# Optimization experiments

Measured on AMD Instinct MI355X. Metric: run time of the kernel, lower is better.

## Reference

```python
import jax, jax.numpy as jnp
import numpy as np

B, L, S = 128, 400, 30
V, EMB, H, M, OOV = 50000, 128, 512, 512, 30


def setup_inputs():
    ks = jax.random.split(jax.random.key(0), 32)
    rn = lambda k, s, sc=0.05: jax.random.normal(k, s, dtype=jnp.float32) * sc
    return {
        "h": rn(ks[0], (1, B, H), 1.0),
        "word_memory_bank": rn(ks[1], (B, L, M), 1.0),
        "sent_memory_bank": rn(ks[2], (B, S, M), 1.0),
        "src_word_mask": (jax.random.uniform(ks[3], (B, L)) < 0.9).astype(jnp.float32),
        "src_sent_mask": (jax.random.uniform(ks[4], (B, S)) < 0.9).astype(jnp.float32),
        "coverage": jnp.zeros((B, L), jnp.float32),
        "emb_table": rn(ks[5], (V, EMB), 1.0).at[0].set(0.0),  # pad_idx=0 row zeroed
        "gru_w_ih": rn(ks[6], (3 * H, EMB)),
        "gru_w_hh": rn(ks[7], (3 * H, H)),
        "gru_b_ih": rn(ks[8], (3 * H,)),
        "gru_b_hh": rn(ks[9], (3 * H,)),
        "w_mem_proj": rn(ks[10], (H, M)),
        "w_dec_proj_w": rn(ks[11], (H, H)),
        "w_dec_proj_b": rn(ks[12], (H,)),
        "w_v": rn(ks[13], (H,)),
        "w_cov_proj": rn(ks[14], (H,)),
        "s_mem_proj": rn(ks[15], (H, M)),
        "s_dec_proj_w": rn(ks[16], (H, H)),
        "s_dec_proj_b": rn(ks[17], (H,)),
        "s_v": rn(ks[18], (H,)),
        "pgen_w": rn(ks[19], (EMB + H + 2 * M,)),
        "pgen_b": rn(ks[20], (1,)),
        "vd1_w": rn(ks[21], (H, H + 2 * M)),
        "vd1_b": rn(ks[22], (H,)),
        "vd2_w": rn(ks[23], (V, H)),
        "vd2_b": rn(ks[24], (V,)),
        "y": jax.random.randint(ks[25], (B,), 0, V),
        "src_oov": jax.random.randint(ks[26], (B, L), 0, V + OOV),
        "max_num_oovs": OOV,
    }


def _attn_concat(dec, mem, mask, mem_proj, dec_w, dec_b, v, cov=None, cov_proj=None):
    # concat/Bahdanau attention: score = v^T tanh(W_m m + W_d s [+ W_c c])
    feat = jnp.einsum('blm,dm->bld', mem, mem_proj) + (dec @ dec_w.T + dec_b)[:, None, :]
    if cov is not None:
        feat = feat + cov[:, :, None] * cov_proj[None, None, :]
    scores = jnp.einsum('bld,d->bl', jnp.tanh(feat), v)
    attn = jax.nn.softmax(scores, axis=1)
    if mask is not None:  # masked softmax: softmax, mask, renormalize
        attn = attn * mask
        attn = attn / (jnp.sum(attn, axis=1, keepdims=True) + 1e-10)
    ctx = jnp.einsum('bl,blm->bm', attn, mem)
    new_cov = cov + attn if cov is not None else None
    return ctx, attn, new_cov


def _forward(h, word_memory_bank, sent_memory_bank, src_word_mask, src_sent_mask,
             coverage, emb_table, gru_w_ih, gru_w_hh, gru_b_ih, gru_b_hh,
             w_mem_proj, w_dec_proj_w, w_dec_proj_b, w_v, w_cov_proj,
             s_mem_proj, s_dec_proj_w, s_dec_proj_b, s_v,
             pgen_w, pgen_b, vd1_w, vd1_b, vd2_w, vd2_b, y, src_oov, max_num_oovs):
    bsz = src_oov.shape[0]
    y_emb = emb_table[y]  # [B, EMB]
    # single-step GRU (PyTorch gate layout r,z,n)
    gi = y_emb @ gru_w_ih.T + gru_b_ih
    gh = h[-1] @ gru_w_hh.T + gru_b_hh
    ir, iz, inn = jnp.split(gi, 3, axis=1)
    hr, hz, hn = jnp.split(gh, 3, axis=1)
    r = jax.nn.sigmoid(ir + hr)
    z = jax.nn.sigmoid(iz + hz)
    n = jnp.tanh(inn + r * hn)
    h_last = (1.0 - z) * n + z * h[-1]  # [B, H]
    h_next = h_last[None]  # [1, B, H]
    word_ctx, word_attn, word_cov = _attn_concat(
        h_last, word_memory_bank, src_word_mask, w_mem_proj, w_dec_proj_w,
        w_dec_proj_b, w_v, coverage, w_cov_proj)
    sent_ctx, _, _ = _attn_concat(
        h_last, sent_memory_bank, src_sent_mask, s_mem_proj, s_dec_proj_w,
        s_dec_proj_b, s_v)
    context = jnp.concatenate([word_ctx, sent_ctx], axis=1)  # [B, 2M]
    hid = jnp.concatenate([context, h_last], axis=1) @ vd1_w.T + vd1_b
    vocab_dist = jax.nn.softmax(hid @ vd2_w.T + vd2_b, axis=1)  # [B, V]
    pg_in = jnp.concatenate([context, h_last, y_emb], axis=1)
    p_gen = jax.nn.sigmoid(pg_in @ pgen_w + pgen_b)[:, None]  # [B, 1]
    vocab_dist_ = p_gen * vocab_dist
    attn_dist_ = (1.0 - p_gen) * word_attn
    vocab_dist_ = jnp.concatenate(
        [vocab_dist_, jnp.zeros((bsz, max_num_oovs), vocab_dist_.dtype)], axis=1)
    final_dist = vocab_dist_.at[jnp.arange(bsz)[:, None], src_oov].add(attn_dist_)
    return final_dist, h_next, word_ctx, word_attn, p_gen, word_cov


def reference(h, word_memory_bank, sent_memory_bank, src_word_mask, src_sent_mask,
              coverage, emb_table, gru_w_ih, gru_w_hh, gru_b_ih, gru_b_hh,
              w_mem_proj, w_dec_proj_w, w_dec_proj_b, w_v, w_cov_proj,
              s_mem_proj, s_dec_proj_w, s_dec_proj_b, s_v,
              pgen_w, pgen_b, vd1_w, vd1_b, vd2_w, vd2_b, y, src_oov, max_num_oovs):
    return _forward(h, word_memory_bank, sent_memory_bank, src_word_mask,
                    src_sent_mask, coverage, emb_table, gru_w_ih, gru_w_hh,
                    gru_b_ih, gru_b_hh, w_mem_proj, w_dec_proj_w, w_dec_proj_b,
                    w_v, w_cov_proj, s_mem_proj, s_dec_proj_w, s_dec_proj_b,
                    s_v, pgen_w, pgen_b, vd1_w, vd1_b, vd2_w, vd2_b,
                    y, src_oov, max_num_oovs)
```

## Files before the change

kernel.cpp:

```cpp
#include <hip/hip_runtime.h>
#include <hip/hip_bf16.h>
#include <math.h>

#define B 128
#define L 400
#define S 30
#define V 50000
#define EMB 128
#define H 512
#define M 512
#define OOV 30
#define H3 1536
#define VO (V + OOV)

#define O_HN    (B * VO)
#define O_WCTX  (O_HN + B * H)
#define O_WATTN (O_WCTX + B * M)
#define O_PGEN  (O_WATTN + B * L)
#define O_WCOV  (O_PGEN + B)

typedef short bf16x8 __attribute__((ext_vector_type(8)));
typedef float f32x4 __attribute__((ext_vector_type(4)));

__device__ __forceinline__ unsigned pk2(float a, float b) {
    union { __hip_bfloat162 h; unsigned u; } cv;
    cv.h = __float22bfloat162_rn(make_float2(a, b));
    return cv.u;
}

__device__ __forceinline__ float fast_tanh(float x) {
    float e = __expf(2.f * x);
    return 1.f - 2.f * __builtin_amdgcn_rcpf(e + 1.f);
}

__global__ void k_setup(const float* __restrict__ bih, const float* __restrict__ bhh,
                        const float* __restrict__ bdpw, const float* __restrict__ bdps,
                        const float* __restrict__ v1b, const float* __restrict__ emb,
                        const int* __restrict__ y,
                        float* gi, float* gh, float* dpw, float* dps, float* hid,
                        float* wscore, float* sscore, float* yemb,
                        const float* __restrict__ wih, const float* __restrict__ whh,
                        const float* __restrict__ wdpw, const float* __restrict__ wdps,
                        const float* __restrict__ wmpw, const float* __restrict__ wmps,
                        const float* __restrict__ v1,
                        short* o_ih, short* o_hh, short* o_dpw, short* o_dps,
                        short* o_mpw, short* o_mps, short* o_v1) {
    int bb = blockIdx.x;
    if (bb < 2583) {
        int i = bb * 256 + threadIdx.x;
        if (i < 196608) { gi[i] = bih[i % 1536]; return; }
        i -= 196608;
        if (i < 196608) { gh[i] = bhh[i % 1536]; return; }
        i -= 196608;
        if (i < 65536) { dpw[i] = bdpw[i & 511]; return; }
        i -= 65536;
        if (i < 65536) { dps[i] = bdps[i & 511]; return; }
        i -= 65536;
        if (i < 65536) { hid[i] = v1b[i & 511]; return; }
        i -= 65536;
        if (i < 51200) { wscore[i] = 0.f; return; }
        i -= 51200;
        if (i < 3840) { sscore[i] = 0.f; return; }
        i -= 3840;
        if (i < 16384) { int b = i >> 7, e = i & 127; yemb[i] = emb[(size_t)y[b] * EMB + e]; }
        return;
    }
    bb -= 2583;
    const float* src; short* dst;
    if      (bb < 96)  { src = wih;  dst = o_ih; }
    else if (bb < 480) { src = whh;  dst = o_hh;  bb -= 96; }
    else if (bb < 608) { src = wdpw; dst = o_dpw; bb -= 480; }
    else if (bb < 736) { src = wdps; dst = o_dps; bb -= 608; }
    else if (bb < 864) { src = wmpw; dst = o_mpw; bb -= 736; }
    else if (bb < 992) { src = wmps; dst = o_mps; bb -= 864; }
    else               { src = v1;   dst = o_v1;  bb -= 992; }
    size_t i = (size_t)bb * 2048 + threadIdx.x * 8;
    float4 a = *(const float4*)(src + i);
    float4 c = *(const float4*)(src + i + 4);
    uint4 w;
    w.x = pk2(a.x, a.y); w.y = pk2(a.z, a.w);
    w.z = pk2(c.x, c.y); w.w = pk2(c.z, c.w);
    *(uint4*)(dst + i) = w;
}

__device__ __forceinline__ void stage_a(const float* __restrict__ src, int SK, int rmax,
                                        int t, short dst[128][72]) {
    int col = (t & 7) * 8;
    int r0 = t >> 3;
#pragma unroll
    for (int i = 0; i < 4; ++i) {
        int r = r0 + i * 32;
        int rr = r < rmax ? r : rmax;
        const float* p = src + (size_t)rr * SK + col;
        float4 a = *(const float4*)p;
        float4 c = *(const float4*)(p + 4);
        uint4 w;
        w.x = pk2(a.x, a.y); w.y = pk2(a.z, a.w);
        w.z = pk2(c.x, c.y); w.w = pk2(c.z, c.w);
        *(uint4*)&dst[r][col] = w;
    }
}

__device__ __forceinline__ void stage_b128bf(const short* __restrict__ src, int K,
                                             int t, short dst[128][72]) {
    int col = (t & 7) * 8;
    int r0 = t >> 3;
#pragma unroll
    for (int i = 0; i < 4; ++i) {
        int r = r0 + i * 32;
        *(bf16x8*)&dst[r][col] = *(const bf16x8*)(src + (size_t)r * K + col);
    }
}

__global__ __launch_bounds__(256, 2) void k_mmsk(
        const float* __restrict__ A0, const short* __restrict__ B0, float* __restrict__ C0,
        int K0, int NT0, int KB0,
        const float* __restrict__ A1, const short* __restrict__ B1, float* __restrict__ C1,
        int K1, int NT1, int KB1) {
    __shared__ short As[128][72];
    __shared__ short Bs[128][72];
    int t = threadIdx.x, lane = t & 63, wv = t >> 6;
    int wr = wv >> 1, wc = wv & 1;
    int l15 = lane & 15, l4 = lane >> 4;

    int bb = blockIdx.x;
    const float* A; const short* Bb; float* C; int K, NT, KB;
    if (bb < NT0 * KB0) { A = A0; Bb = B0; C = C0; K = K0; NT = NT0; KB = KB0; }
    else { bb -= NT0 * KB0; A = A1; Bb = B1; C = C1; K = K1; NT = NT1; KB = KB1; }
    int nIdx = bb % NT, kIdx = bb / NT;
    int ldc = NT * 128;
    int nBase = nIdx * 128;
    int KC = K / KB;
    int kLo = kIdx * KC, kHi = kLo + KC;

    f32x4 acc[4][4] = {};
    for (int kc = kLo; kc < kHi; kc += 64) {
        stage_a(A + kc, K, 127, t, As);
        stage_b128bf(Bb + (size_t)nBase * K + kc, K, t, Bs);
        __syncthreads();
#pragma unroll
        for (int kk = 0; kk < 2; ++kk) {
            bf16x8 af[4], bq[4];
#pragma unroll
            for (int i = 0; i < 4; ++i)
                af[i] = *(const bf16x8*)&As[wr * 64 + i * 16 + l15][kk * 32 + l4 * 8];
#pragma unroll
            for (int j = 0; j < 4; ++j)
                bq[j] = *(const bf16x8*)&Bs[wc * 64 + j * 16 + l15][kk * 32 + l4 * 8];
#pragma unroll
            for (int i = 0; i < 4; ++i)
#pragma unroll
                for (int j = 0; j < 4; ++j)
                    acc[i][j] = __builtin_amdgcn_mfma_f32_16x16x32_bf16(
                        af[i], bq[j], acc[i][j], 0, 0, 0);
        }
        __syncthreads();
    }
#pragma unroll
    for (int i = 0; i < 4; ++i)
#pragma unroll
        for (int r = 0; r < 4; ++r) {
            int row = wr * 64 + i * 16 + l4 * 4 + r;
#pragma unroll
            for (int j = 0; j < 4; ++j) {
                int n = nBase + wc * 64 + j * 16 + l15;
                atomicAdd(&C[(size_t)row * ldc + n], acc[i][j][r]);
            }
        }
}

__global__ __launch_bounds__(256, 2) void k_mm128(
        const float* __restrict__ Ap, const float* __restrict__ Bf,
        const float* __restrict__ bias, float* __restrict__ C, int K, int ldc, int Nlim) {
    __shared__ short As[128][72];
    __shared__ short Bs[128][72];
    int t = threadIdx.x, lane = t & 63, wv = t >> 6;
    int wr = wv >> 1, wc = wv & 1;
    int l15 = lane & 15, l4 = lane >> 4;
    int nBase = blockIdx.x * 128;
    int brmax = Nlim - 1 - nBase; if (brmax > 127) brmax = 127;

    f32x4 acc[4][4] = {};
    for (int kc = 0; kc < K; kc += 64) {
        stage_a(Ap + kc, K, 127, t, As);
        stage_a(Bf + (size_t)nBase * K + kc, K, brmax, t, Bs);
        __syncthreads();
#pragma unroll
        for (int kk = 0; kk < 2; ++kk) {
            bf16x8 af[4], bq[4];
#pragma unroll
            for (int i = 0; i < 4; ++i)
                af[i] = *(const bf16x8*)&As[wr * 64 + i * 16 + l15][kk * 32 + l4 * 8];
#pragma unroll
            for (int j = 0; j < 4; ++j)
                bq[j] = *(const bf16x8*)&Bs[wc * 64 + j * 16 + l15][kk * 32 + l4 * 8];
#pragma unroll
            for (int i = 0; i < 4; ++i)
#pragma unroll
                for (int j = 0; j < 4; ++j)
                    acc[i][j] = __builtin_amdgcn_mfma_f32_16x16x32_bf16(
                        af[i], bq[j], acc[i][j], 0, 0, 0);
        }
        __syncthreads();
    }
#pragma unroll
    for (int i = 0; i < 4; ++i)
#pragma unroll
        for (int r = 0; r < 4; ++r) {
            int row = wr * 64 + i * 16 + l4 * 4 + r;
#pragma unroll
            for (int j = 0; j < 4; ++j) {
                int n = nBase + wc * 64 + j * 16 + l15;
                if (n < Nlim) C[(size_t)row * ldc + n] = acc[i][j][r] + bias[n];
            }
        }
}

__global__ __launch_bounds__(256, 4) void k_feat(
        const float* __restrict__ wmb, const short* __restrict__ wbmpw,
        const float* __restrict__ dpw, const float* __restrict__ cov,
        const float* __restrict__ covp, const float* __restrict__ vw,
        float* __restrict__ wscore,
        const float* __restrict__ smb, const short* __restrict__ wbmps,
        const float* __restrict__ dps, const float* __restrict__ vs,
        float* __restrict__ sscore) {
    __shared__ short As[128][72];
    __shared__ short Bs[128][72];
    int t = threadIdx.x, lane = t & 63, wv = t >> 6;
    int wr = wv >> 1, wc = wv & 1;
    int l15 = lane & 15, l4 = lane >> 4;

    bool word = blockIdx.y < 400;
    const float* Ap; const short* Bbf; const float* dproj; const float* vvec; float* outp;
    int rowBase;
    if (word) { Ap = wmb; Bbf = wbmpw; dproj = dpw; vvec = vw; outp = wscore; rowBase = blockIdx.y * 128; }
    else      { Ap = smb; Bbf = wbmps; dproj = dps; vvec = vs; outp = sscore; rowBase = (blockIdx.y - 400) * 128; }
    int nBase = blockIdx.x * 128;
    const float* Asrc = Ap + (size_t)rowBase * 512;
    const short* Bsrc = Bbf + (size_t)nBase * 512;

    f32x4 acc[4][4] = {};
    for (int kc = 0; kc < 512; kc += 64) {
        stage_a(Asrc + kc, 512, 127, t, As);
        stage_b128bf(Bsrc + kc, 512, t, Bs);
        __syncthreads();
#pragma unroll
        for (int kk = 0; kk < 2; ++kk) {
            bf16x8 af[4], bq[4];
#pragma unroll
            for (int i = 0; i < 4; ++i)
                af[i] = *(const bf16x8*)&As[wr * 64 + i * 16 + l15][kk * 32 + l4 * 8];
#pragma unroll
            for (int j = 0; j < 4; ++j)
                bq[j] = *(const bf16x8*)&Bs[wc * 64 + j * 16 + l15][kk * 32 + l4 * 8];
#pragma unroll
            for (int i = 0; i < 4; ++i)
#pragma unroll
                for (int j = 0; j < 4; ++j)
                    acc[i][j] = __builtin_amdgcn_mfma_f32_16x16x32_bf16(
                        af[i], bq[j], acc[i][j], 0, 0, 0);
        }
        __syncthreads();
    }
    int dB = nBase + wc * 64;
    float vv[4], cp[4];
#pragma unroll
    for (int j = 0; j < 4; ++j) {
        int d = dB + j * 16 + l15;
        vv[j] = vvec[d];
        cp[j] = word ? covp[d] : 0.f;
    }
#pragma unroll
    for (int i = 0; i < 4; ++i) {
#pragma unroll
        for (int r = 0; r < 4; ++r) {
            int row = rowBase + wr * 64 + i * 16 + l4 * 4 + r;
            int b = word ? (row / 400) : (row / 30);
            float cv = word ? cov[row] : 0.f;
            float s = 0.f;
#pragma unroll
            for (int j = 0; j < 4; ++j) {
                float dpv = dproj[b * H + dB + j * 16 + l15];
                float f = acc[i][j][r] + dpv + cv * cp[j];
                s += vv[j] * fast_tanh(f);
            }
            s += __shfl_xor(s, 8, 16);
            s += __shfl_xor(s, 4, 16);
            s += __shfl_xor(s, 2, 16);
            s += __shfl_xor(s, 1, 16);
            if (l15 == 0) atomicAdd(&outp[row], s);
        }
    }
}

__global__ void k_gates(const float* __restrict__ gi, const float* __restrict__ gh,
                        const float* __restrict__ h, float* __restrict__ hnext) {
    int i = blockIdx.x * 256 + threadIdx.x;
    int b = i >> 9, k = i & 511;
    float ir = gi[b * H3 + k], iz = gi[b * H3 + H + k], inn = gi[b * H3 + 2 * H + k];
    float hr = gh[b * H3 + k], hz = gh[b * H3 + H + k], hn = gh[b * H3 + 2 * H + k];
    float r = 1.f / (1.f + __expf(-(ir + hr)));
    float z = 1.f / (1.f + __expf(-(iz + hz)));
    float n = fast_tanh(inn + r * hn);
    hnext[i] = (1.f - z) * n + z * h[i];
}

__global__ __launch_bounds__(256) void k_smax_sent(
        const float* __restrict__ wscore, const float* __restrict__ wmask,
        const float* __restrict__ cov, float* __restrict__ wattn, float* __restrict__ wcov,
        const float* __restrict__ sscore, const float* __restrict__ smask,
        const float* __restrict__ smb, float* __restrict__ sctx) {
    __shared__ float sc[L];
    __shared__ float red[4];
    int t = threadIdx.x;
    if (blockIdx.x < B) {
        int b = blockIdx.x;
        float mx = -1e30f;
        for (int l = t; l < L; l += 256) { float s = wscore[b * L + l]; sc[l] = s; mx = fmaxf(mx, s); }
        for (int off = 32; off; off >>= 1) mx = fmaxf(mx, __shfl_xor(mx, off));
        if ((t & 63) == 0) red[t >> 6] = mx;
        __syncthreads();
        mx = fmaxf(fmaxf(red[0], red[1]), fmaxf(red[2], red[3]));
        __syncthreads();
        float sm = 0.f;
        for (int l = t; l < L; l += 256) { float e = __expf(sc[l] - mx); sc[l] = e; sm += e; }
        for (int off = 32; off; off >>= 1) sm += __shfl_xor(sm, off);
        if ((t & 63) == 0) red[t >> 6] = sm;
        __syncthreads();
        float Z = red[0] + red[1] + red[2] + red[3];
        __syncthreads();
        float sm2 = 0.f;
        for (int l = t; l < L; l += 256) {
            float a = (sc[l] / Z) * wmask[b * L + l];
            sc[l] = a; sm2 += a;
        }
        for (int off = 32; off; off >>= 1) sm2 += __shfl_xor(sm2, off);
        if ((t & 63) == 0) red[t >> 6] = sm2;
        __syncthreads();
        float Zm = red[0] + red[1] + red[2] + red[3] + 1e-10f;
        for (int l = t; l < L; l += 256) {
            float a = sc[l] / Zm;
            wattn[b * L + l] = a;
            wcov[b * L + l] = cov[b * L + l] + a;
        }
    } else {
        int b = blockIdx.x - B;
        float* sa = sc; float* sa2 = sc + 32; float* smk = sc + 64;
        if (t < S) { sa[t] = sscore[b * S + t]; smk[t] = smask[b * S + t]; }
        __syncthreads();
        if (t < S) {
            float mx = -1e30f;
            for (int l = 0; l < S; ++l) mx = fmaxf(mx, sa[l]);
            float Z = 0.f, Zm = 0.f;
            for (int l = 0; l < S; ++l) { float e = __expf(sa[l] - mx); Z += e; Zm += e * smk[l]; }
            float e = __expf(sa[t] - mx);
            float a = (e / Z) * smk[t];
            sa2[t] = a / (Zm / Z + 1e-10f);
        }
        __syncthreads();
        float a0 = 0.f, a1 = 0.f;
        for (int l = 0; l < S; ++l) {
            const float* r = smb + ((size_t)b * S + l) * M;
            float a = sa2[l];
            a0 += a * r[t]; a1 += a * r[t + 256];
        }
        sctx[b * M + t] = a0; sctx[b * M + t + 256] = a1;
    }
}

__global__ __launch_bounds__(256) void k_ctx_part(
        const float* __restrict__ attn, const float* __restrict__ memb,
        float* __restrict__ ctxp) {
    __shared__ float sa[100];
    int b = blockIdx.y, ch = blockIdx.x, t = threadIdx.x;
    int l0 = ch * 100;
    if (t < 100) sa[t] = attn[b * L + l0 + t];
    __syncthreads();
    float ax = 0.f, ay = 0.f;
    const float* base = memb + ((size_t)b * L + l0) * M + t * 2;
#pragma unroll 4
    for (int l = 0; l < 100; ++l) {
        float2 m2 = *(const float2*)(base + (size_t)l * M);
        float a = sa[l];
        ax += a * m2.x; ay += a * m2.y;
    }
    float* o = ctxp + ((size_t)(ch * B + b)) * M + t * 2;
    o[0] = ax; o[1] = ay;
}

__global__ void k_ctxcat(const float* __restrict__ ctxp, const float* __restrict__ sctx,
                         const float* __restrict__ hnext, const float* __restrict__ yemb,
                         const float* __restrict__ pw, const float* __restrict__ pb,
                         float* __restrict__ wctx, float* __restrict__ cat,
                         float* __restrict__ pg) {
    int bb = blockIdx.x, t = threadIdx.x;
    if (bb < 256) {
        int j = bb * 256 + t;
        float v = ctxp[j] + ctxp[B * M + j] + ctxp[2 * B * M + j] + ctxp[3 * B * M + j];
        wctx[j] = v;
        int b = j >> 9, c = j & 511;
        cat[b * H3 + c] = v;
    } else if (bb < 768) {
        int i = (bb - 256) * 256 + t;
        int b = i >> 10, c = i & 1023;
        cat[b * H3 + 512 + c] = (c < 512) ? sctx[b * 512 + c] : hnext[b * 512 + c - 512];
    } else {
        int b = bb - 768;
        if (t < 64) {
            float s = 0.f;
            for (int i = t; i < EMB + H + 2 * M; i += 64) {
                float x;
                if (i < 512) {
                    int j = b * 512 + i;
                    x = ctxp[j] + ctxp[B * M + j] + ctxp[2 * B * M + j] + ctxp[3 * B * M + j];
                } else if (i < 1024) x = sctx[b * 512 + i - 512];
                else if (i < 1536)   x = hnext[b * 512 + i - 1024];
                else                 x = yemb[b * EMB + i - 1536];
                s += x * pw[i];
            }
            for (int off = 32; off; off >>= 1) s += __shfl_xor(s, off);
            if (t == 0) pg[b] = 1.f / (1.f + __expf(-(s + pb[0])));
        }
    }
}

__global__ __launch_bounds__(256) void k_vpart(
        const float* __restrict__ logits, float* __restrict__ pm, float* __restrict__ ps) {
    __shared__ float wm[4], wsv[4];
    int b = blockIdx.y, c = blockIdx.x, t = threadIdx.x;
    const float4* row = (const float4*)(logits + (size_t)b * V) + c * 1250;
    float m = -3e38f, s = 0.f;
    for (int i = t; i < 1250; i += 256) {
        float4 x = row[i];
        float m4 = fmaxf(fmaxf(x.x, x.y), fmaxf(x.z, x.w));
        if (m4 > m) { s *= __expf(m - m4); m = m4; }
        s += __expf(x.x - m) + __expf(x.y - m) + __expf(x.z - m) + __expf(x.w - m);
    }
    for (int off = 32; off; off >>= 1) {
        float mo = __shfl_xor(m, off), so = __shfl_xor(s, off);
        float mn = fmaxf(m, mo);
        s = s * __expf(m - mn) + so * __expf(mo - mn);
        m = mn;
    }
    if ((t & 63) == 0) { wm[t >> 6] = m; wsv[t >> 6] = s; }
    __syncthreads();
    if (t == 0) {
        float M2 = fmaxf(fmaxf(wm[0], wm[1]), fmaxf(wm[2], wm[3]));
        float S2 = wsv[0] * __expf(wm[0] - M2) + wsv[1] * __expf(wm[1] - M2) +
                   wsv[2] * __expf(wm[2] - M2) + wsv[3] * __expf(wm[3] - M2);
        pm[b * 10 + c] = M2; ps[b * 10 + c] = S2;
    }
}

__global__ __launch_bounds__(256) void k_vwrite(
        const float* __restrict__ logits, const float* __restrict__ pm,
        const float* __restrict__ ps, const float* __restrict__ pgen,
        float* __restrict__ fd) {
    int b = blockIdx.y, t = threadIdx.x;
    float M2 = -3e38f;
#pragma unroll
    for (int c = 0; c < 10; ++c) M2 = fmaxf(M2, pm[b * 10 + c]);
    float S2 = 0.f;
#pragma unroll
    for (int c = 0; c < 10; ++c) S2 += ps[b * 10 + c] * __expf(pm[b * 10 + c] - M2);
    float inv = pgen[b] / S2;
    int col0 = blockIdx.x * 2048 + t * 8;
    float* outb = fd + (size_t)b * VO;
    if (col0 + 8 <= V) {
        const float4* lp = (const float4*)(logits + (size_t)b * V + col0);
        float4 x = lp[0], z = lp[1];
        *(float2*)(outb + col0)     = make_float2(inv * __expf(x.x - M2), inv * __expf(x.y - M2));
        *(float2*)(outb + col0 + 2) = make_float2(inv * __expf(x.z - M2), inv * __expf(x.w - M2));
        *(float2*)(outb + col0 + 4) = make_float2(inv * __expf(z.x - M2), inv * __expf(z.y - M2));
        *(float2*)(outb + col0 + 6) = make_float2(inv * __expf(z.z - M2), inv * __expf(z.w - M2));
    } else {
#pragma unroll
        for (int k = 0; k < 8; k += 2) {
            int c = col0 + k;
            if (c + 2 <= VO) {
                float2 o;
                o.x = (c < V)     ? inv * __expf(logits[(size_t)b * V + c] - M2) : 0.f;
                o.y = (c + 1 < V) ? inv * __expf(logits[(size_t)b * V + c + 1] - M2) : 0.f;
                *(float2*)(outb + c) = o;
            }
        }
    }
}

__global__ void k_scatter(const int* __restrict__ oov, const float* __restrict__ wattn,
                          const float* __restrict__ pgen, float* __restrict__ fd) {
    int i = blockIdx.x * 256 + threadIdx.x;
    int b = i / L;
    float w = (1.f - pgen[b]) * wattn[i];
    atomicAdd(&fd[(size_t)b * VO + oov[i]], w);
}

extern "C" void kernel_launch(void* const* d_in, const int* in_sizes, int n_in,
                              void* d_out, int out_size, void* d_ws, size_t ws_size,
                              hipStream_t stream) {
    const float* h     = (const float*)d_in[0];
    const float* wmb   = (const float*)d_in[1];
    const float* smb   = (const float*)d_in[2];
    const float* wmask = (const float*)d_in[3];
    const float* smask = (const float*)d_in[4];
    const float* cov   = (const float*)d_in[5];
    const float* emb   = (const float*)d_in[6];
    const float* Wih   = (const float*)d_in[7];
    const float* Whh   = (const float*)d_in[8];
    const float* bih   = (const float*)d_in[9];
    const float* bhh   = (const float*)d_in[10];
    const float* Wmpw  = (const float*)d_in[11];
    const float* Wdpw  = (const float*)d_in[12];
    const float* bdpw  = (const float*)d_in[13];
    const float* vw    = (const float*)d_in[14];
    const float* covp  = (const float*)d_in[15];
    const float* Wmps  = (const float*)d_in[16];
    const float* Wdps  = (const float*)d_in[17];
    const float* bdps  = (const float*)d_in[18];
    const float* vs    = (const float*)d_in[19];
    const float* pw    = (const float*)d_in[20];
    const float* pb    = (const float*)d_in[21];
    const float* vd1w  = (const float*)d_in[22];
    const float* vd1b  = (const float*)d_in[23];
    const float* vd2w  = (const float*)d_in[24];
    const float* vd2b  = (const float*)d_in[25];
    const int*   y     = (const int*)d_in[26];
    const int*   oov   = (const int*)d_in[27];

    float* out   = (float*)d_out;
    float* fd    = out;
    float* hnext = out + O_HN;
    float* wctx  = out + O_WCTX;
    float* wattn = out + O_WATTN;
    float* pgen  = out + O_PGEN;
    float* wcov  = out + O_WCOV;

    float* ws     = (float*)d_ws;
    float* yemb   = ws;
    float* gi     = yemb + B * EMB;
    float* gh     = gi + B * H3;
    float* dpw    = gh + B * H3;
    float* dps    = dpw + B * H;
    float* wscore = dps + B * H;
    float* sscore = wscore + B * L;
    float* sctx   = sscore + B * S;
    float* hid    = sctx + B * M;
    float* logits = hid + B * H;
    float* cat    = gi;
    float* ctxp   = logits;
    short* wb     = (short*)(logits + (size_t)B * V);
    short* wb_ih  = wb;
    short* wb_hh  = wb_ih + H3 * EMB;
    short* wb_dpw = wb_hh + H3 * H;
    short* wb_dps = wb_dpw + H * H;
    short* wb_mpw = wb_dps + H * H;
    short* wb_mps = wb_mpw + H * M;
    short* wb_v1  = wb_mps + H * M;
    float* pm     = (float*)(wb_v1 + H * H3);
    float* psum   = pm + B * 10;

    k_setup<<<2583 + 1376, 256, 0, stream>>>(bih, bhh, bdpw, bdps, vd1b, emb, y,
                                             gi, gh, dpw, dps, hid, wscore, sscore, yemb,
                                             Wih, Whh, Wdpw, Wdps, Wmpw, Wmps, vd1w,
                                             wb_ih, wb_hh, wb_dpw, wb_dps, wb_mpw, wb_mps, wb_v1);
    k_mmsk<<<36, 256, 0, stream>>>(yemb, wb_ih, gi, 128, 12, 1,
                                   h, wb_hh, gh, 512, 12, 2);
    k_gates<<<256, 256, 0, stream>>>(gi, gh, h, hnext);
    k_mmsk<<<16, 256, 0, stream>>>(hnext, wb_dpw, dpw, 512, 4, 2,
                                   hnext, wb_dps, dps, 512, 4, 2);
    k_feat<<<dim3(4, 430), 256, 0, stream>>>(wmb, wb_mpw, dpw, cov, covp, vw, wscore,
                                             smb, wb_mps, dps, vs, sscore);
    k_smax_sent<<<2 * B, 256, 0, stream>>>(wscore, wmask, cov, wattn, wcov,
                                           sscore, smask, smb, sctx);
    k_ctx_part<<<dim3(4, B), 256, 0, stream>>>(wattn, wmb, ctxp);
    k_ctxcat<<<768 + B, 256, 0, stream>>>(ctxp, sctx, hnext, yemb, pw, pb,
                                          wctx, cat, pgen);
    k_mmsk<<<24, 256, 0, stream>>>(cat, wb_v1, hid, 1536, 4, 6,
                                   nullptr, nullptr, nullptr, 64, 1, 0);
    k_mm128<<<(V + 127) / 128, 256, 0, stream>>>(hid, vd2w, vd2b, logits, H, V, V);
    k_vpart<<<dim3(10, B), 256, 0, stream>>>(logits, pm, psum);
    k_vwrite<<<dim3(25, B), 256, 0, stream>>>(logits, pm, psum, pgen, fd);
    k_scatter<<<200, 256, 0, stream>>>(oov, wattn, pgen, fd);
}
```

Measured before the change: 265.0 us.

## Pre-convert memory banks to swizzled bf16 tiles and load via global_load_lds

Adds conversion blocks, piggybacked onto the early small GEMM launches, that convert the fp32 word and sentence memory banks and the projection weights into bf16 tiles with an XOR swizzle. A new feature kernel then streams those tiles straight into LDS with global_load_lds and uses a 256-wide N tile with cached decoder-projection values. This removes the in-loop fp32-to-bf16 staging and halves the A re-reads across N tiles. The cost is an extra full write and read of the memory bank in bf16 and a larger workspace, with a fallback kernel when the workspace is too small. k_mm128's occupancy hint is also raised.

```diff
diff --git a/kernel.cpp b/kernel.cpp
--- a/kernel.cpp
+++ b/kernel.cpp
@@ -31,6 +31,12 @@
 __device__ __forceinline__ float fast_tanh(float x) {
     float e = __expf(2.f * x);
     return 1.f - 2.f * __builtin_amdgcn_rcpf(e + 1.f);
+}
+
+__device__ __forceinline__ void gload16(const void* g, void* l) {
+    __builtin_amdgcn_global_load_lds(
+        (const __attribute__((address_space(1))) unsigned int*)g,
+        (__attribute__((address_space(3))) unsigned int*)l, 16, 0, 0);
 }
 
 __global__ void k_setup(const float* __restrict__ bih, const float* __restrict__ bhh,
@@ -83,6 +89,23 @@
     *(uint4*)(dst + i) = w;
 }
 
+__device__ __forceinline__ void cvt_granule(const float* __restrict__ src,
+                                            short* __restrict__ dst,
+                                            int gidx, int TRlog) {
+    int TR = 1 << TRlog;
+    int g = gidx & 7;
+    int r = (gidx >> 3) & (TR - 1);
+    int kc = (gidx >> (3 + TRlog)) & 7;
+    int tile = gidx >> (6 + TRlog);
+    const float* p = src + (size_t)(tile * TR + r) * 512 + kc * 64 + ((g ^ (r & 7)) << 3);
+    float4 a = *(const float4*)p;
+    float4 c = *(const float4*)(p + 4);
+    uint4 w;
+    w.x = pk2(a.x, a.y); w.y = pk2(a.z, a.w);
+    w.z = pk2(c.x, c.y); w.w = pk2(c.z, c.w);
+    *(uint4*)(dst + (size_t)gidx * 8) = w;
+}
+
 __device__ __forceinline__ void stage_a(const float* __restrict__ src, int SK, int rmax,
                                         int t, short dst[128][72]) {
     int col = (t & 7) * 8;
@@ -112,14 +135,36 @@
     }
 }
 
+__device__ __forceinline__ void stage_b256bf(const short* __restrict__ src, int K,
+                                             int t, short dst[256][72]) {
+    int col = (t & 7) * 8;
+    int r0 = t >> 3;
+#pragma unroll
+    for (int i = 0; i < 8; ++i) {
+        int r = r0 + i * 32;
+        *(bf16x8*)&dst[r][col] = *(const bf16x8*)(src + (size_t)r * K + col);
+    }
+}
+
 __global__ __launch_bounds__(256, 2) void k_mmsk(
         const float* __restrict__ A0, const short* __restrict__ B0, float* __restrict__ C0,
         int K0, int NT0, int KB0,
         const float* __restrict__ A1, const short* __restrict__ B1, float* __restrict__ C1,
-        int K1, int NT1, int KB1) {
+        int K1, int NT1, int KB1,
+        int gemmBlocks,
+        const float* __restrict__ cs0, short* __restrict__ cd0, int ntile0,
+        const float* __restrict__ cs1, short* __restrict__ cd1, int TRlog) {
     __shared__ short As[128][72];
     __shared__ short Bs[128][72];
-    int t = threadIdx.x, lane = t & 63, wv = t >> 6;
+    int t = threadIdx.x;
+    if ((int)blockIdx.x >= gemmBlocks) {
+        int gidx = ((int)blockIdx.x - gemmBlocks) * 256 + t;
+        int split = ntile0 * (64 << TRlog);
+        if (gidx < split) cvt_granule(cs0, cd0, gidx, TRlog);
+        else              cvt_granule(cs1, cd1, gidx - split, TRlog);
+        return;
+    }
+    int lane = t & 63, wv = t >> 6;
     int wr = wv >> 1, wc = wv & 1;
     int l15 = lane & 15, l4 = lane >> 4;
 
@@ -169,7 +214,7 @@
         }
 }
 
-__global__ __launch_bounds__(256, 2) void k_mm128(
+__global__ __launch_bounds__(256, 4) void k_mm128(
         const float* __restrict__ Ap, const float* __restrict__ Bf,
         const float* __restrict__ bias, float* __restrict__ C, int K, int ldc, int Nlim) {
     __shared__ short As[128][72];
@@ -216,7 +261,105 @@
         }
 }
 
-__global__ __launch_bounds__(256, 4) void k_feat(
+__global__ __launch_bounds__(256, 2) void k_feat_g(
+        const short* __restrict__ wmb_t, const short* __restrict__ wmp_t,
+        const float* __restrict__ dpw, const float* __restrict__ cov,
+        const float* __restrict__ covp, const float* __restrict__ vw,
+        float* __restrict__ wscore,
+        const short* __restrict__ smb_t, const short* __restrict__ smp_t,
+        const float* __restrict__ dps, const float* __restrict__ vs,
+        float* __restrict__ sscore) {
+    __shared__ alignas(16) short As[128 * 64];
+    __shared__ alignas(16) short Bs[256 * 64];
+    int t = threadIdx.x, lane = t & 63, wv = t >> 6;
+    int wr = wv >> 1, wc = wv & 1;
+    int l15 = lane & 15, l4 = lane >> 4;
+
+    bool word = blockIdx.y < 400;
+    const short* At; const short* Bt; const float* dproj; const float* vvec; float* outp;
+    int tile;
+    if (word) { At = wmb_t; Bt = wmp_t; dproj = dpw; vvec = vw; outp = wscore; tile = blockIdx.y; }
+    else      { At = smb_t; Bt = smp_t; dproj = dps; vvec = vs; outp = sscore; tile = blockIdx.y - 400; }
+    int rowBase = tile * 128;
+    int nT = blockIdx.x;
+    int nBase = nT * 256;
+    const short* Abase = At + (size_t)tile * 65536;
+    const short* Bbase = Bt + (size_t)nT * 131072;
+
+    f32x4 acc[4][8] = {};
+    int swz = l15 & 7;
+    for (int kc = 0; kc < 8; ++kc) {
+        const char* Ab = (const char*)(Abase + kc * 8192);
+        const char* Bb = (const char*)(Bbase + kc * 16384);
+        char* AsB = (char*)As;
+        char* BsB = (char*)Bs;
+#pragma unroll
+        for (int it = 0; it < 4; ++it) {
+            int lo = wv * 4096 + it * 1024;
+            gload16(Ab + lo + lane * 16, AsB + lo);
+        }
+#pragma unroll
+        for (int it = 0; it < 8; ++it) {
+            int lo = wv * 8192 + it * 1024;
+            gload16(Bb + lo + lane * 16, BsB + lo);
+        }
+        __syncthreads();
+#pragma unroll
+        for (int kk = 0; kk < 2; ++kk) {
+            int g = ((kk * 4 + l4) ^ swz) * 8;
+            bf16x8 af[4], bq[8];
+#pragma unroll
+            for (int i = 0; i < 4; ++i)
+                af[i] = *(const bf16x8*)&As[(wr * 64 + i * 16 + l15) * 64 + g];
+#pragma unroll
+            for (int j = 0; j < 8; ++j)
+                bq[j] = *(const bf16x8*)&Bs[(wc * 128 + j * 16 + l15) * 64 + g];
+#pragma unroll
+            for (int i = 0; i < 4; ++i)
+#pragma unroll
+                for (int j = 0; j < 8; ++j)
+                    acc[i][j] = __builtin_amdgcn_mfma_f32_16x16x32_bf16(
+                        af[i], bq[j], acc[i][j], 0, 0, 0);
+        }
+        __syncthreads();
+    }
+    int dB = nBase + wc * 128;
+    float vv[8], cp[8], dp0[8], dp1[8];
+    int b0 = word ? rowBase / 400 : 0;
+    int b1 = word ? (rowBase + 127) / 400 : 0;
+#pragma unroll
+    for (int j = 0; j < 8; ++j) {
+        int d = dB + j * 16 + l15;
+        vv[j] = vvec[d];
+        cp[j] = word ? covp[d] : 0.f;
+        if (word) { dp0[j] = dproj[b0 * H + d]; dp1[j] = dproj[b1 * H + d]; }
+    }
+#pragma unroll
+    for (int i = 0; i < 4; ++i) {
+#pragma unroll
+        for (int r = 0; r < 4; ++r) {
+            int row = rowBase + wr * 64 + i * 16 + l4 * 4 + r;
+            int b = word ? (row / 400) : (row / 30);
+            float cv = word ? cov[row] : 0.f;
+            bool use0 = (b == b0);
+            float s = 0.f;
+#pragma unroll
+            for (int j = 0; j < 8; ++j) {
+                float dpv = word ? (use0 ? dp0[j] : dp1[j])
+                                 : dproj[b * H + dB + j * 16 + l15];
+                float f = acc[i][j][r] + dpv + cv * cp[j];
+                s += vv[j] * fast_tanh(f);
+            }
+            s += __shfl_xor(s, 8, 16);
+            s += __shfl_xor(s, 4, 16);
+            s += __shfl_xor(s, 2, 16);
+            s += __shfl_xor(s, 1, 16);
+            if (l15 == 0) atomicAdd(&outp[row], s);
+        }
+    }
+}
+
+__global__ __launch_bounds__(256, 2) void k_feat2(
         const float* __restrict__ wmb, const short* __restrict__ wbmpw,
         const float* __restrict__ dpw, const float* __restrict__ cov,
         const float* __restrict__ covp, const float* __restrict__ vw,
@@ -225,7 +368,7 @@
         const float* __restrict__ dps, const float* __restrict__ vs,
         float* __restrict__ sscore) {
     __shared__ short As[128][72];
-    __shared__ short Bs[128][72];
+    __shared__ short Bs[256][72];
     int t = threadIdx.x, lane = t & 63, wv = t >> 6;
     int wr = wv >> 1, wc = wv & 1;
     int l15 = lane & 15, l4 = lane >> 4;
@@ -235,40 +378,43 @@
     int rowBase;
     if (word) { Ap = wmb; Bbf = wbmpw; dproj = dpw; vvec = vw; outp = wscore; rowBase = blockIdx.y * 128; }
     else      { Ap = smb; Bbf = wbmps; dproj = dps; vvec = vs; outp = sscore; rowBase = (blockIdx.y - 400) * 128; }
-    int nBase = blockIdx.x * 128;
+    int nBase = blockIdx.x * 256;
     const float* Asrc = Ap + (size_t)rowBase * 512;
     const short* Bsrc = Bbf + (size_t)nBase * 512;
 
-    f32x4 acc[4][4] = {};
+    f32x4 acc[4][8] = {};
     for (int kc = 0; kc < 512; kc += 64) {
         stage_a(Asrc + kc, 512, 127, t, As);
-        stage_b128bf(Bsrc + kc, 512, t, Bs);
+        stage_b256bf(Bsrc + kc, 512, t, Bs);
         __syncthreads();
 #pragma unroll
         for (int kk = 0; kk < 2; ++kk) {
-            bf16x8 af[4], bq[4];
+            bf16x8 af[4], bq[8];
 #pragma unroll
             for (int i = 0; i < 4; ++i)
                 af[i] = *(const bf16x8*)&As[wr * 64 + i * 16 + l15][kk * 32 + l4 * 8];
 #pragma unroll
-            for (int j = 0; j < 4; ++j)
-                bq[j] = *(const bf16x8*)&Bs[wc * 64 + j * 16 + l15][kk * 32 + l4 * 8];
+            for (int j = 0; j < 8; ++j)
+                bq[j] = *(const bf16x8*)&Bs[wc * 128 + j * 16 + l15][kk * 32 + l4 * 8];
 #pragma unroll
             for (int i = 0; i < 4; ++i)
 #pragma unroll
-                for (int j = 0; j < 4; ++j)
+                for (int j = 0; j < 8; ++j)
                     acc[i][j] = __builtin_amdgcn_mfma_f32_16x16x32_bf16(
                         af[i], bq[j], acc[i][j], 0, 0, 0);
         }
         __syncthreads();
     }
-    int dB = nBase + wc * 64;
-    float vv[4], cp[4];
-#pragma unroll
-    for (int j = 0; j < 4; ++j) {
+    int dB = nBase + wc * 128;
+    float vv[8], cp[8], dp0[8], dp1[8];
+    int b0 = word ? rowBase / 400 : 0;
+    int b1 = word ? (rowBase + 127) / 400 : 0;
+#pragma unroll
+    for (int j = 0; j < 8; ++j) {
         int d = dB + j * 16 + l15;
         vv[j] = vvec[d];
         cp[j] = word ? covp[d] : 0.f;
+        if (word) { dp0[j] = dproj[b0 * H + d]; dp1[j] = dproj[b1 * H + d]; }
     }
 #pragma unroll
     for (int i = 0; i < 4; ++i) {
@@ -277,10 +423,12 @@
             int row = rowBase + wr * 64 + i * 16 + l4 * 4 + r;
             int b = word ? (row / 400) : (row / 30);
             float cv = word ? cov[row] : 0.f;
+            bool use0 = (b == b0);
             float s = 0.f;
 #pragma unroll
-            for (int j = 0; j < 4; ++j) {
-                float dpv = dproj[b * H + dB + j * 16 + l15];
+            for (int j = 0; j < 8; ++j) {
+                float dpv = word ? (use0 ? dp0[j] : dp1[j])
+                                 : dproj[b * H + dB + j * 16 + l15];
                 float f = acc[i][j][r] + dpv + cv * cp[j];
                 s += vv[j] * fast_tanh(f);
             }
@@ -558,25 +706,40 @@
     short* wb_v1  = wb_mps + H * M;
     float* pm     = (float*)(wb_v1 + H * H3);
     float* psum   = pm + B * 10;
+    short* wmb_t  = (short*)(psum + B * 10);
+    short* smb_t  = wmb_t + 400 * 65536;
+    short* wmp_t  = smb_t + 30 * 65536;
+    short* smp_t  = wmp_t + 2 * 131072;
+    size_t NEED = (size_t)((char*)(smp_t + 2 * 131072) - (char*)d_ws);
+    bool big = ws_size >= NEED;
 
     k_setup<<<2583 + 1376, 256, 0, stream>>>(bih, bhh, bdpw, bdps, vd1b, emb, y,
                                              gi, gh, dpw, dps, hid, wscore, sscore, yemb,
                                              Wih, Whh, Wdpw, Wdps, Wmpw, Wmps, vd1w,
                                              wb_ih, wb_hh, wb_dpw, wb_dps, wb_mpw, wb_mps, wb_v1);
-    k_mmsk<<<36, 256, 0, stream>>>(yemb, wb_ih, gi, 128, 12, 1,
-                                   h, wb_hh, gh, 512, 12, 2);
+    int cvt1 = big ? 13760 : 0;
+    k_mmsk<<<36 + cvt1, 256, 0, stream>>>(yemb, wb_ih, gi, 128, 12, 1,
+                                          h, wb_hh, gh, 512, 12, 2,
+                                          36, wmb, wmb_t, 400, smb, smb_t, 7);
     k_gates<<<256, 256, 0, stream>>>(gi, gh, h, hnext);
-    k_mmsk<<<16, 256, 0, stream>>>(hnext, wb_dpw, dpw, 512, 4, 2,
-                                   hnext, wb_dps, dps, 512, 4, 2);
-    k_feat<<<dim3(4, 430), 256, 0, stream>>>(wmb, wb_mpw, dpw, cov, covp, vw, wscore,
-                                             smb, wb_mps, dps, vs, sscore);
+    int cvt2 = big ? 256 : 0;
+    k_mmsk<<<16 + cvt2, 256, 0, stream>>>(hnext, wb_dpw, dpw, 512, 4, 2,
+                                          hnext, wb_dps, dps, 512, 4, 2,
+                                          16, Wmpw, wmp_t, 2, Wmps, smp_t, 8);
+    if (big)
+        k_feat_g<<<dim3(2, 430), 256, 0, stream>>>(wmb_t, wmp_t, dpw, cov, covp, vw, wscore,
+                                                   smb_t, smp_t, dps, vs, sscore);
+    else
+        k_feat2<<<dim3(2, 430), 256, 0, stream>>>(wmb, wb_mpw, dpw, cov, covp, vw, wscore,
+                                                  smb, wb_mps, dps, vs, sscore);
     k_smax_sent<<<2 * B, 256, 0, stream>>>(wscore, wmask, cov, wattn, wcov,
                                            sscore, smask, smb, sctx);
     k_ctx_part<<<dim3(4, B), 256, 0, stream>>>(wattn, wmb, ctxp);
     k_ctxcat<<<768 + B, 256, 0, stream>>>(ctxp, sctx, hnext, yemb, pw, pb,
                                           wctx, cat, pgen);
     k_mmsk<<<24, 256, 0, stream>>>(cat, wb_v1, hid, 1536, 4, 6,
-                                   nullptr, nullptr, nullptr, 64, 1, 0);
+                                   nullptr, nullptr, nullptr, 64, 1, 0,
+                                   24, nullptr, nullptr, 0, nullptr, nullptr, 0);
     k_mm128<<<(V + 127) / 128, 256, 0, stream>>>(hid, vd2w, vd2b, logits, H, V, V);
     k_vpart<<<dim3(10, B), 256, 0, stream>>>(logits, pm, psum);
     k_vwrite<<<dim3(25, B), 256, 0, stream>>>(logits, pm, psum, pgen, fd);
```

Result: faster. 232.8 us (-12.1%).

## Fuse vocab softmax partials into logits GEMM and widen attention feature tiles

Applied to the files above, without the earlier changes.

The vocab GEMM epilogue now computes per-row max and sum-exp partials for each 64-column slice and writes them out. This removes the separate k_vpart pass that re-read the full logits matrix, and k_vwrite now combines the 782 partials per row itself. Separately, k_feat uses 256-wide N tiles with register-prefetched, software-pipelined loads, and hoists the decoder-projection loads for the at most two batches a tile spans. The trade-offs are more combine work repeated in every k_vwrite block, higher register pressure in k_feat (occupancy hint lowered to 2), and a raised occupancy hint on k_mm128.

```diff
diff --git a/kernel.cpp b/kernel.cpp
--- a/kernel.cpp
+++ b/kernel.cpp
@@ -12,6 +12,9 @@
 #define OOV 30
 #define H3 1536
 #define VO (V + OOV)
+#define NTILE 391
+#define NPART (2 * NTILE)
+#define PSTRIDE 800
 
 #define O_HN    (B * VO)
 #define O_WCTX  (O_HN + B * H)
@@ -169,21 +172,22 @@
         }
 }
 
-__global__ __launch_bounds__(256, 2) void k_mm128(
+__global__ __launch_bounds__(256, 4) void k_mm128(
         const float* __restrict__ Ap, const float* __restrict__ Bf,
-        const float* __restrict__ bias, float* __restrict__ C, int K, int ldc, int Nlim) {
+        const float* __restrict__ bias, float* __restrict__ C,
+        float* __restrict__ pm, float* __restrict__ ps) {
     __shared__ short As[128][72];
     __shared__ short Bs[128][72];
     int t = threadIdx.x, lane = t & 63, wv = t >> 6;
     int wr = wv >> 1, wc = wv & 1;
     int l15 = lane & 15, l4 = lane >> 4;
     int nBase = blockIdx.x * 128;
-    int brmax = Nlim - 1 - nBase; if (brmax > 127) brmax = 127;
+    int brmax = V - 1 - nBase; if (brmax > 127) brmax = 127;
 
     f32x4 acc[4][4] = {};
-    for (int kc = 0; kc < K; kc += 64) {
-        stage_a(Ap + kc, K, 127, t, As);
-        stage_a(Bf + (size_t)nBase * K + kc, K, brmax, t, Bs);
+    for (int kc = 0; kc < H; kc += 64) {
+        stage_a(Ap + kc, H, 127, t, As);
+        stage_a(Bf + (size_t)nBase * H + kc, H, brmax, t, Bs);
         __syncthreads();
 #pragma unroll
         for (int kk = 0; kk < 2; ++kk) {
@@ -208,15 +212,39 @@
 #pragma unroll
         for (int r = 0; r < 4; ++r) {
             int row = wr * 64 + i * 16 + l4 * 4 + r;
+            float val[4];
+            float mrow = -3e38f;
 #pragma unroll
             for (int j = 0; j < 4; ++j) {
                 int n = nBase + wc * 64 + j * 16 + l15;
-                if (n < Nlim) C[(size_t)row * ldc + n] = acc[i][j][r] + bias[n];
-            }
-        }
-}
-
-__global__ __launch_bounds__(256, 4) void k_feat(
+                val[j] = acc[i][j][r] + bias[n < V ? n : 0];
+                if (n < V) {
+                    C[(size_t)row * V + n] = val[j];
+                    mrow = fmaxf(mrow, val[j]);
+                }
+            }
+            float srow = 0.f;
+#pragma unroll
+            for (int j = 0; j < 4; ++j) {
+                int n = nBase + wc * 64 + j * 16 + l15;
+                if (n < V) srow += __expf(val[j] - mrow);
+            }
+#pragma unroll
+            for (int off = 1; off < 16; off <<= 1) {
+                float mo = __shfl_xor(mrow, off, 16), so = __shfl_xor(srow, off, 16);
+                float mn = fmaxf(mrow, mo);
+                srow = srow * __expf(mrow - mn) + so * __expf(mo - mn);
+                mrow = mn;
+            }
+            if (l15 == 0) {
+                int idx = blockIdx.x * 2 + wc;
+                pm[row * PSTRIDE + idx] = mrow;
+                ps[row * PSTRIDE + idx] = srow;
+            }
+        }
+}
+
+__global__ __launch_bounds__(256, 2) void k_feat(
         const float* __restrict__ wmb, const short* __restrict__ wbmpw,
         const float* __restrict__ dpw, const float* __restrict__ cov,
         const float* __restrict__ covp, const float* __restrict__ vw,
@@ -225,7 +253,7 @@
         const float* __restrict__ dps, const float* __restrict__ vs,
         float* __restrict__ sscore) {
     __shared__ short As[128][72];
-    __shared__ short Bs[128][72];
+    __shared__ short Bs[256][72];
     int t = threadIdx.x, lane = t & 63, wv = t >> 6;
     int wr = wv >> 1, wc = wv & 1;
     int l15 = lane & 15, l4 = lane >> 4;
@@ -235,40 +263,75 @@
     int rowBase;
     if (word) { Ap = wmb; Bbf = wbmpw; dproj = dpw; vvec = vw; outp = wscore; rowBase = blockIdx.y * 128; }
     else      { Ap = smb; Bbf = wbmps; dproj = dps; vvec = vs; outp = sscore; rowBase = (blockIdx.y - 400) * 128; }
-    int nBase = blockIdx.x * 128;
+    int nBase = blockIdx.x * 256;
     const float* Asrc = Ap + (size_t)rowBase * 512;
     const short* Bsrc = Bbf + (size_t)nBase * 512;
 
-    f32x4 acc[4][4] = {};
-    for (int kc = 0; kc < 512; kc += 64) {
-        stage_a(Asrc + kc, 512, 127, t, As);
-        stage_b128bf(Bsrc + kc, 512, t, Bs);
-        __syncthreads();
+    int col = (t & 7) * 8;
+    int r0 = t >> 3;
+
+    float4 pa[4][2];
+    bf16x8 pb[8];
+    auto loadA = [&](int kc) {
+#pragma unroll
+        for (int i = 0; i < 4; ++i) {
+            const float* p = Asrc + (size_t)(r0 + i * 32) * 512 + kc * 64 + col;
+            pa[i][0] = *(const float4*)p;
+            pa[i][1] = *(const float4*)(p + 4);
+        }
+    };
+    auto loadB = [&](int kc) {
+#pragma unroll
+        for (int i = 0; i < 8; ++i)
+            pb[i] = *(const bf16x8*)(Bsrc + (size_t)(r0 + i * 32) * 512 + kc * 64 + col);
+    };
+    auto writeLDS = [&]() {
+#pragma unroll
+        for (int i = 0; i < 4; ++i) {
+            uint4 w;
+            w.x = pk2(pa[i][0].x, pa[i][0].y); w.y = pk2(pa[i][0].z, pa[i][0].w);
+            w.z = pk2(pa[i][1].x, pa[i][1].y); w.w = pk2(pa[i][1].z, pa[i][1].w);
+            *(uint4*)&As[r0 + i * 32][col] = w;
+        }
+#pragma unroll
+        for (int i = 0; i < 8; ++i)
+            *(bf16x8*)&Bs[r0 + i * 32][col] = pb[i];
+    };
+
+    f32x4 acc[4][8] = {};
+    loadA(0); loadB(0);
+    for (int kc = 0; kc < 8; ++kc) {
+        writeLDS();
+        __syncthreads();
+        if (kc < 7) { loadA(kc + 1); loadB(kc + 1); }
 #pragma unroll
         for (int kk = 0; kk < 2; ++kk) {
-            bf16x8 af[4], bq[4];
+            bf16x8 af[4], bq[8];
 #pragma unroll
             for (int i = 0; i < 4; ++i)
                 af[i] = *(const bf16x8*)&As[wr * 64 + i * 16 + l15][kk * 32 + l4 * 8];
 #pragma unroll
-            for (int j = 0; j < 4; ++j)
-                bq[j] = *(const bf16x8*)&Bs[wc * 64 + j * 16 + l15][kk * 32 + l4 * 8];
+            for (int j = 0; j < 8; ++j)
+                bq[j] = *(const bf16x8*)&Bs[wc * 128 + j * 16 + l15][kk * 32 + l4 * 8];
 #pragma unroll
             for (int i = 0; i < 4; ++i)
 #pragma unroll
-                for (int j = 0; j < 4; ++j)
+                for (int j = 0; j < 8; ++j)
                     acc[i][j] = __builtin_amdgcn_mfma_f32_16x16x32_bf16(
                         af[i], bq[j], acc[i][j], 0, 0, 0);
         }
         __syncthreads();
     }
-    int dB = nBase + wc * 64;
-    float vv[4], cp[4];
-#pragma unroll
-    for (int j = 0; j < 4; ++j) {
+    int dB = nBase + wc * 128;
+    float vv[8], cp[8], dp0[8], dp1[8];
+    int b0 = word ? rowBase / 400 : 0;
+    int b1 = word ? (rowBase + 127) / 400 : 0;
+#pragma unroll
+    for (int j = 0; j < 8; ++j) {
         int d = dB + j * 16 + l15;
         vv[j] = vvec[d];
         cp[j] = word ? covp[d] : 0.f;
+        if (word) { dp0[j] = dproj[b0 * H + d]; dp1[j] = dproj[b1 * H + d]; }
     }
 #pragma unroll
     for (int i = 0; i < 4; ++i) {
@@ -277,10 +340,12 @@
             int row = rowBase + wr * 64 + i * 16 + l4 * 4 + r;
             int b = word ? (row / 400) : (row / 30);
             float cv = word ? cov[row] : 0.f;
+            bool use0 = (b == b0);
             float s = 0.f;
 #pragma unroll
-            for (int j = 0; j < 4; ++j) {
-                float dpv = dproj[b * H + dB + j * 16 + l15];
+            for (int j = 0; j < 8; ++j) {
+                float dpv = word ? (use0 ? dp0[j] : dp1[j])
+                                 : dproj[b * H + dB + j * 16 + l15];
                 float f = acc[i][j][r] + dpv + cv * cp[j];
                 s += vv[j] * fast_tanh(f);
             }
@@ -424,17 +489,18 @@
     }
 }
 
-__global__ __launch_bounds__(256) void k_vpart(
-        const float* __restrict__ logits, float* __restrict__ pm, float* __restrict__ ps) {
+__global__ __launch_bounds__(256) void k_vwrite(
+        const float* __restrict__ logits, const float* __restrict__ pm,
+        const float* __restrict__ ps, const float* __restrict__ pgen,
+        float* __restrict__ fd) {
     __shared__ float wm[4], wsv[4];
-    int b = blockIdx.y, c = blockIdx.x, t = threadIdx.x;
-    const float4* row = (const float4*)(logits + (size_t)b * V) + c * 1250;
+    int b = blockIdx.y, t = threadIdx.x;
     float m = -3e38f, s = 0.f;
-    for (int i = t; i < 1250; i += 256) {
-        float4 x = row[i];
-        float m4 = fmaxf(fmaxf(x.x, x.y), fmaxf(x.z, x.w));
-        if (m4 > m) { s *= __expf(m - m4); m = m4; }
-        s += __expf(x.x - m) + __expf(x.y - m) + __expf(x.z - m) + __expf(x.w - m);
+    for (int i = t; i < NPART; i += 256) {
+        float mo = pm[b * PSTRIDE + i], so = ps[b * PSTRIDE + i];
+        float mn = fmaxf(m, mo);
+        s = s * __expf(m - mn) + so * __expf(mo - mn);
+        m = mn;
     }
     for (int off = 32; off; off >>= 1) {
         float mo = __shfl_xor(m, off), so = __shfl_xor(s, off);
@@ -444,25 +510,9 @@
     }
     if ((t & 63) == 0) { wm[t >> 6] = m; wsv[t >> 6] = s; }
     __syncthreads();
-    if (t == 0) {
-        float M2 = fmaxf(fmaxf(wm[0], wm[1]), fmaxf(wm[2], wm[3]));
-        float S2 = wsv[0] * __expf(wm[0] - M2) + wsv[1] * __expf(wm[1] - M2) +
-                   wsv[2] * __expf(wm[2] - M2) + wsv[3] * __expf(wm[3] - M2);
-        pm[b * 10 + c] = M2; ps[b * 10 + c] = S2;
-    }
-}
-
-__global__ __launch_bounds__(256) void k_vwrite(
-        const float* __restrict__ logits, const float* __restrict__ pm,
-        const float* __restrict__ ps, const float* __restrict__ pgen,
-        float* __restrict__ fd) {
-    int b = blockIdx.y, t = threadIdx.x;
-    float M2 = -3e38f;
-#pragma unroll
-    for (int c = 0; c < 10; ++c) M2 = fmaxf(M2, pm[b * 10 + c]);
-    float S2 = 0.f;
-#pragma unroll
-    for (int c = 0; c < 10; ++c) S2 += ps[b * 10 + c] * __expf(pm[b * 10 + c] - M2);
+    float M2 = fmaxf(fmaxf(wm[0], wm[1]), fmaxf(wm[2], wm[3]));
+    float S2 = wsv[0] * __expf(wm[0] - M2) + wsv[1] * __expf(wm[1] - M2) +
+               wsv[2] * __expf(wm[2] - M2) + wsv[3] * __expf(wm[3] - M2);
     float inv = pgen[b] / S2;
     int col0 = blockIdx.x * 2048 + t * 8;
     float* outb = fd + (size_t)b * VO;
@@ -557,7 +607,7 @@
     short* wb_mps = wb_mpw + H * M;
     short* wb_v1  = wb_mps + H * M;
     float* pm     = (float*)(wb_v1 + H * H3);
-    float* psum   = pm + B * 10;
+    float* psum   = pm + B * PSTRIDE;
 
     k_setup<<<2583 + 1376, 256, 0, stream>>>(bih, bhh, bdpw, bdps, vd1b, emb, y,
                                              gi, gh, dpw, dps, hid, wscore, sscore, yemb,
@@ -568,7 +618,7 @@
     k_gates<<<256, 256, 0, stream>>>(gi, gh, h, hnext);
     k_mmsk<<<16, 256, 0, stream>>>(hnext, wb_dpw, dpw, 512, 4, 2,
                                    hnext, wb_dps, dps, 512, 4, 2);
-    k_feat<<<dim3(4, 430), 256, 0, stream>>>(wmb, wb_mpw, dpw, cov, covp, vw, wscore,
+    k_feat<<<dim3(2, 430), 256, 0, stream>>>(wmb, wb_mpw, dpw, cov, covp, vw, wscore,
                                              smb, wb_mps, dps, vs, sscore);
     k_smax_sent<<<2 * B, 256, 0, stream>>>(wscore, wmask, cov, wattn, wcov,
                                            sscore, smask, smb, sctx);
@@ -577,8 +627,7 @@
                                           wctx, cat, pgen);
     k_mmsk<<<24, 256, 0, stream>>>(cat, wb_v1, hid, 1536, 4, 6,
                                    nullptr, nullptr, nullptr, 64, 1, 0);
-    k_mm128<<<(V + 127) / 128, 256, 0, stream>>>(hid, vd2w, vd2b, logits, H, V, V);
-    k_vpart<<<dim3(10, B), 256, 0, stream>>>(logits, pm, psum);
+    k_mm128<<<NTILE, 256, 0, stream>>>(hid, vd2w, vd2b, logits, pm, psum);
     k_vwrite<<<dim3(25, B), 256, 0, stream>>>(logits, pm, psum, pgen, fd);
     k_scatter<<<200, 256, 0, stream>>>(oov, wattn, pgen, fd);
 }
```

After: 220.1 us (median of 2 runs). 1.2x faster.
